# Performance work log

Measured on AMD Instinct MI355X. Metric: run time of the kernel, lower is better.

## Reference

```python
import jax, jax.numpy as jnp
import numpy as np

# --- the 9 fixed 3x3x3 planar structuring elements from MorphPool3D.__init__ ---
def _make_offsets():
    P = [np.zeros((3, 3, 3), np.int8) for _ in range(9)]
    P[0][:, :, 1] = 1
    P[1][:, 1, :] = 1
    P[2][1, :, :] = 1
    P[3][:, [0, 1, 2], [0, 1, 2]] = 1
    P[4][:, [0, 1, 2], [2, 1, 0]] = 1
    P[5][[0, 1, 2], :, [0, 1, 2]] = 1
    P[6][[0, 1, 2], :, [2, 1, 0]] = 1
    P[7][[0, 1, 2], [0, 1, 2], :] = 1
    P[8][[0, 1, 2], [2, 1, 0], :] = 1
    # list of [9,3] integer offsets relative to the 3x3x3 center (all masks are
    # point-symmetric, so scipy's structure reflection in dilation is a no-op)
    return [np.argwhere(m) - 1 for m in P]

_OFFSETS = _make_offsets()


def _morph_chain(x, red):
    """Sequentially apply all 9 structuring elements with reduction `red`.

    red = jnp.minimum -> composed binary erosions (scipy border_value=0 -> pad 0)
    red = jnp.maximum -> composed binary dilations (border_value=0   -> pad 0)
    Note: the original appends the SAME (in-place mutated) numpy array each
    iteration, so its max/min over 'layers' is a no-op; the net effect is the
    sequential composition over all 9 masks, which is what we compute here.
    x: [B, 1, D, H, W] binary float.
    """
    D, H, W = x.shape[-3:]
    for offs in _OFFSETS:
        xp = jnp.pad(x, ((0, 0), (0, 0), (1, 1), (1, 1), (1, 1)))  # zeros
        acc = None
        for di, dj, dk in offs:
            s = xp[:, :, 1 + di:1 + di + D, 1 + dj:1 + dj + H, 1 + dk:1 + dk + W]
            acc = s if acc is None else red(acc, s)
        x = acc
    return x


def _forward(inp, aux):
    # aux thresholding (MorphPoolFunction.forward), then binarize (scipy
    # binary_erosion/dilation treat any nonzero as True)
    t = jnp.where(aux < 0, jnp.ones((), inp.dtype),
                  jnp.where(aux > 0, jnp.zeros((), inp.dtype), inp))
    b = (t != 0).astype(inp.dtype)
    # Fcycle alternates per batch element starting at index 0:
    #   even i: inf_sup(sup_inf(x)) = erode_all(dilate_all(x))  (close-like)
    #   odd  i: sup_inf(inf_sup(x)) = dilate_all(erode_all(x))  (open-like)
    close = _morph_chain(_morph_chain(b, jnp.maximum), jnp.minimum)
    open_ = _morph_chain(_morph_chain(b, jnp.minimum), jnp.maximum)
    B = inp.shape[0]
    even = (jnp.arange(B) % 2 == 0).reshape(B, 1, 1, 1, 1)
    return jnp.where(even, close, open_)


def setup_inputs() -> dict:
    key = jax.random.key(0)
    k1, k2 = jax.random.split(key)
    B, C, D, H, W = 4, 1, 160, 160, 160
    inp = jax.random.uniform(k1, (B, C, D, H, W), dtype=jnp.float32)
    aux = jax.random.normal(k2, (B, C, D, H, W), dtype=jnp.float32)
    return {"input": inp, "aux": aux, "device": 0}


def reference(input, aux, device):
    del device  # CUDA device id in the original; irrelevant here
    return _forward(input, aux)
```

## Files before the change

### kernel.cpp

```cpp
#include <hip/hip_runtime.h>
#include <cstdint>

typedef unsigned long long u64;

constexpr int S   = 160;
constexpr int NB  = 4;
constexpr int PAD = 8;
constexpr int SP  = S + 2 * PAD;
constexpr int BUFW = NB * SP * 3 * SP;
constexpr int BLKC = 512;

__device__ __forceinline__ int widx(int b, int dp, int w, int hp) {
  return ((b * SP + dp) * 3 + w) * SP + hp;
}

struct R3 { u64 a, b, c; };

template <bool OR_> __device__ __forceinline__ u64 rop(u64 x, u64 y) { return OR_ ? (x | y) : (x & y); }
template <bool OR_> __device__ __forceinline__ R3 rop3(R3 x, R3 y) {
  return {rop<OR_>(x.a, y.a), rop<OR_>(x.b, y.b), rop<OR_>(x.c, y.c)};
}
template <int N> __device__ __forceinline__ R3 sl3(R3 x) {
  return {x.a << N, (x.b << N) | (x.a >> (64 - N)), (x.c << N) | (x.b >> (64 - N))};
}
template <int N> __device__ __forceinline__ R3 sr3(R3 x) {
  return {(x.a >> N) | (x.b << (64 - N)), (x.b >> N) | (x.c << (64 - N)), x.c >> N};
}
template <bool OR_> __device__ __forceinline__ R3 e1(R3 x) {
  return rop3<OR_>(rop3<OR_>(x, sl3<1>(x)), sr3<1>(x));
}
__device__ __forceinline__ R3 ldr(const u64* p) { return {p[0], p[1], p[2]}; }

template <bool OR_, bool TOOUT>
__device__ void chain_body(const u64* __restrict__ src, u64* __restrict__ dstBits,
                           float* __restrict__ out, int b, int d0, int h0,
                           u64* sIN, u64* sT1, u64* sT2) {
  for (int i = threadIdx.x; i < 32 * 32 * 3; i += BLKC) {
    const int hi = i % 32, w = (i / 32) % 3, di = i / 96;
    sIN[(di * 32 + hi) * 3 + w] = src[widx(b, d0 + di, w, h0 + hi)];
  }
  __syncthreads();

  for (int s = threadIdx.x; s < 32 * 20; s += BLKC) {
    const int dd = s / 20, hh = s % 20;
    const u64* base = sIN + (dd * 32 + hh) * 3;
    R3 G1 = ldr(base + 2 * 3);
#pragma unroll
    for (int r = 3; r <= 10; ++r) G1 = rop3<OR_>(G1, ldr(base + r * 3));
    R3 G2 = rop3<OR_>(ldr(base + 1 * 3), ldr(base + 11 * 3));
    R3 G3 = rop3<OR_>(ldr(base + 0 * 3), ldr(base + 12 * 3));
    R3 X = rop3<OR_>(rop3<OR_>(e1<OR_>(e1<OR_>(G1)), e1<OR_>(G2)), G3);
    R3 y = e1<OR_>(X);
    R3 R = rop3<OR_>(rop3<OR_>(y, sl3<3>(y)), sr3<3>(y));
    R.c &= 0xFFFFFFFFull;
    u64* q = sT1 + s * 3; q[0] = R.a; q[1] = R.b; q[2] = R.c;
  }
  __syncthreads();

  for (int s = threadIdx.x; s < 20 * 20; s += BLKC) {
    const int dd = s / 20, hh = s % 20;
    const u64* base = sT1 + (dd * 20 + hh) * 3;
    R3 G1 = ldr(base + 2 * 60);
#pragma unroll
    for (int r = 3; r <= 10; ++r) G1 = rop3<OR_>(G1, ldr(base + r * 60));
    R3 G2 = rop3<OR_>(ldr(base + 1 * 60), ldr(base + 11 * 60));
    R3 G3 = rop3<OR_>(ldr(base + 0 * 60), ldr(base + 12 * 60));
    R3 X = rop3<OR_>(e1<OR_>(rop3<OR_>(e1<OR_>(G1), G2)), G3);
    X.c &= 0xFFFFFFFFull;
    u64* q = sT2 + s * 3; q[0] = X.a; q[1] = X.b; q[2] = X.c;
  }
  __syncthreads();

  if (threadIdx.x < 256) {
    const int s = threadIdx.x;
    const int dd = s >> 4, hh = s & 15;
    const u64* t2 = sT2 + ((dd + 2) * 20 + (hh + 2)) * 3;
    R3 A = ldr(t2);
    A = rop3<OR_>(A, ldr(t2 + (20 + 1) * 3));  A = rop3<OR_>(A, ldr(t2 + (20 - 1) * 3));
    A = rop3<OR_>(A, ldr(t2 - (20 - 1) * 3));  A = rop3<OR_>(A, ldr(t2 - (20 + 1) * 3));
    A = rop3<OR_>(A, ldr(t2 + 40 * 3));        A = rop3<OR_>(A, ldr(t2 - 40 * 3));
    A = rop3<OR_>(A, ldr(t2 + 2 * 3));         A = rop3<OR_>(A, ldr(t2 - 2 * 3));
    A.c &= 0xFFFFFFFFull;
    if (TOOUT) {
      u64* q = sT1 + s * 3;
      q[0] = A.a; q[1] = A.b; q[2] = A.c;
    } else {
      dstBits[widx(b, d0 + dd + PAD, 0, h0 + hh + PAD)] = A.a;
      dstBits[widx(b, d0 + dd + PAD, 1, h0 + hh + PAD)] = A.b;
      dstBits[widx(b, d0 + dd + PAD, 2, h0 + hh + PAD)] = A.c;
    }
  }
  if (TOOUT) {
    __syncthreads();
    for (int q = threadIdx.x; q < 16 * 16 * 40; q += BLKC) {
      const int r = q / 40, j = q % 40;
      const int dd = r >> 4, hh = r & 15;
      const u64 word = sT1[r * 3 + (j >> 4)];
      const unsigned nb = (unsigned)((word >> ((j & 15) * 4)) & 0xFull);
      float4 v;
      v.x = (float)(nb & 1u); v.y = (float)((nb >> 1) & 1u);
      v.z = (float)((nb >> 2) & 1u); v.w = (float)((nb >> 3) & 1u);
      const size_t e = ((size_t)((b * S + d0 + dd) * S + h0 + hh)) * S + j * 4;
      *reinterpret_cast<float4*>(out + e) = v;
    }
  }
}

template <bool PH0, bool TOOUT>
__global__ __launch_bounds__(BLKC) void chain_k(const u64* __restrict__ src,
                                                u64* __restrict__ dstBits,
                                                float* __restrict__ out) {
  __shared__ u64 sIN[32 * 32 * 3];
  __shared__ u64 sT1[32 * 20 * 3];
  __shared__ u64 sT2[20 * 20 * 3];
  const int blk = blockIdx.x;
  const int b = blk / 100, tile = blk % 100;
  const int d0 = (tile / 10) * 16, h0 = (tile % 10) * 16;
  const bool isor = (((b & 1) == 0) == PH0);
  if (isor) chain_body<true , TOOUT>(src, dstBits, out, b, d0, h0, sIN, sT1, sT2);
  else      chain_body<false, TOOUT>(src, dstBits, out, b, d0, h0, sIN, sT1, sT2);
}

__device__ __forceinline__ u64 squash(u64 x) {
  x = (x | (x >> 4))  & 0x00FF00FF00FF00FFull;
  x = (x | (x >> 8))  & 0x0000FFFF0000FFFFull;
  x = (x | (x >> 16)) & 0x00000000FFFFFFFFull;
  return x;
}

__global__ __launch_bounds__(320) void pack_k(const float* __restrict__ aux,
                                              const float* __restrict__ inp,
                                              u64* __restrict__ dstA,
                                              u64* __restrict__ dstB) {
  {
    const int g = blockIdx.x * 320 + threadIdx.x;
    if (g < BUFW) {
      const int hp = g % SP;
      const int dp = (g / (SP * 3)) % SP;
      if ((dp < PAD) | (dp >= S + PAD) | (hp < PAD) | (hp >= S + PAD)) {
        dstA[g] = 0ull; dstB[g] = 0ull;
      }
    }
  }
  __shared__ unsigned char nib[8][48];
  const int r   = threadIdx.x / 40;
  const int pos = threadIdx.x % 40;
  const int row = blockIdx.x * 8 + r;
  const size_t ebase = (size_t)row * S + pos * 4;

  const float4 a = reinterpret_cast<const float4*>(aux)[row * 40 + pos];
  unsigned n = 0;
  if (a.x < 0.0f) n |= 1u; else if (a.x == 0.0f) { if (inp[ebase + 0] != 0.0f) n |= 1u; }
  if (a.y < 0.0f) n |= 2u; else if (a.y == 0.0f) { if (inp[ebase + 1] != 0.0f) n |= 2u; }
  if (a.z < 0.0f) n |= 4u; else if (a.z == 0.0f) { if (inp[ebase + 2] != 0.0f) n |= 4u; }
  if (a.w < 0.0f) n |= 8u; else if (a.w == 0.0f) { if (inp[ebase + 3] != 0.0f) n |= 8u; }
  nib[r][pos] = (unsigned char)n;
  if (threadIdx.x < 64) nib[threadIdx.x >> 3][40 + (threadIdx.x & 7)] = 0;
  __syncthreads();

  if (threadIdx.x < 24) {
    const int rr = threadIdx.x & 7;
    const int w  = threadIdx.x >> 3;
    const u64 x0 = *reinterpret_cast<const u64*>(&nib[rr][w * 16]);
    const u64 x1 = *reinterpret_cast<const u64*>(&nib[rr][w * 16 + 8]);
    const u64 word = squash(x0) | (squash(x1) << 32);
    const int grow = blockIdx.x * 8 + rr;
    const int h = grow % S, d = (grow / S) % S, b = grow / (S * S);
    dstA[widx(b, d + PAD, w, h + PAD)] = word;
  }
}

extern "C" void kernel_launch(void* const* d_in, const int* in_sizes, int n_in,
                              void* d_out, int out_size, void* d_ws, size_t ws_size,
                              hipStream_t stream) {
  (void)in_sizes; (void)n_in; (void)out_size; (void)ws_size;
  const float* inp = (const float*)d_in[0];
  const float* aux = (const float*)d_in[1];
  float* out = (float*)d_out;

  u64* bufA = (u64*)d_ws;
  u64* bufB = bufA + BUFW;

  const int ROWS = NB * S * S;
  pack_k<<<ROWS / 8, 320, 0, stream>>>(aux, inp, bufA, bufB);

  const int CG = NB * 100;
  chain_k<true , false><<<CG, BLKC, 0, stream>>>(bufA, bufB, out);
  chain_k<false, true ><<<CG, BLKC, 0, stream>>>(bufB, bufA, out);
}
```

Measured before the change: 41.19 us.

## Fuse both morphology chain passes into one kernel with a grid barrier

The two chain kernels are merged into one persistent kernel. It runs the first chain, synchronizes all 400 blocks through an atomic counter grid barrier, then runs the second chain. The counter is zeroed inside the pack kernel. This removes one kernel launch and its launch gap. It also switches the aux load and the float output store to nontemporal accesses. The barrier only works if all 400 blocks of 512 threads are co-resident, which holds on MI355X's 256 CUs with the occupancy hint, but a spinning barrier risks deadlock if that fails.

```diff
diff --git a/kernel.cpp b/kernel.cpp
--- a/kernel.cpp
+++ b/kernel.cpp
@@ -2,6 +2,7 @@
 #include <cstdint>
 
 typedef unsigned long long u64;
+typedef float f4 __attribute__((ext_vector_type(4)));
 
 constexpr int S   = 160;
 constexpr int NB  = 4;
@@ -9,6 +10,7 @@
 constexpr int SP  = S + 2 * PAD;
 constexpr int BUFW = NB * SP * 3 * SP;
 constexpr int BLKC = 512;
+constexpr int GRIDC = NB * 100;
 
 __device__ __forceinline__ int widx(int b, int dp, int w, int hp) {
   return ((b * SP + dp) * 3 + w) * SP + hp;
@@ -97,28 +99,44 @@
       const int dd = r >> 4, hh = r & 15;
       const u64 word = sT1[r * 3 + (j >> 4)];
       const unsigned nb = (unsigned)((word >> ((j & 15) * 4)) & 0xFull);
-      float4 v;
+      f4 v;
       v.x = (float)(nb & 1u); v.y = (float)((nb >> 1) & 1u);
       v.z = (float)((nb >> 2) & 1u); v.w = (float)((nb >> 3) & 1u);
       const size_t e = ((size_t)((b * S + d0 + dd) * S + h0 + hh)) * S + j * 4;
-      *reinterpret_cast<float4*>(out + e) = v;
-    }
-  }
-}
-
-template <bool PH0, bool TOOUT>
-__global__ __launch_bounds__(BLKC) void chain_k(const u64* __restrict__ src,
-                                                u64* __restrict__ dstBits,
-                                                float* __restrict__ out) {
+      __builtin_nontemporal_store(v, reinterpret_cast<f4*>(out + e));
+    }
+  }
+}
+
+__global__ __launch_bounds__(BLKC, 4) void mega_k(const u64* __restrict__ bufA,
+                                                  u64* __restrict__ bufB,
+                                                  float* __restrict__ out,
+                                                  unsigned* __restrict__ cnt) {
   __shared__ u64 sIN[32 * 32 * 3];
   __shared__ u64 sT1[32 * 20 * 3];
   __shared__ u64 sT2[20 * 20 * 3];
   const int blk = blockIdx.x;
   const int b = blk / 100, tile = blk % 100;
   const int d0 = (tile / 10) * 16, h0 = (tile % 10) * 16;
-  const bool isor = (((b & 1) == 0) == PH0);
-  if (isor) chain_body<true , TOOUT>(src, dstBits, out, b, d0, h0, sIN, sT1, sT2);
-  else      chain_body<false, TOOUT>(src, dstBits, out, b, d0, h0, sIN, sT1, sT2);
+
+  const bool isorA = ((b & 1) == 0);
+  if (isorA) chain_body<true , false>(bufA, bufB, out, b, d0, h0, sIN, sT1, sT2);
+  else       chain_body<false, false>(bufA, bufB, out, b, d0, h0, sIN, sT1, sT2);
+
+  __syncthreads();
+  if (threadIdx.x == 0) {
+    __threadfence();
+    __hip_atomic_fetch_add(cnt, 1u, __ATOMIC_ACQ_REL, __HIP_MEMORY_SCOPE_AGENT);
+    while (__hip_atomic_load(cnt, __ATOMIC_RELAXED, __HIP_MEMORY_SCOPE_AGENT) < (unsigned)GRIDC) {
+      __builtin_amdgcn_s_sleep(8);
+    }
+    __threadfence();
+  }
+  __syncthreads();
+
+  const bool isorB = ((b & 1) != 0);
+  if (isorB) chain_body<true , true>(bufB, nullptr, out, b, d0, h0, sIN, sT1, sT2);
+  else       chain_body<false, true>(bufB, nullptr, out, b, d0, h0, sIN, sT1, sT2);
 }
 
 __device__ __forceinline__ u64 squash(u64 x) {
@@ -131,9 +149,11 @@
 __global__ __launch_bounds__(320) void pack_k(const float* __restrict__ aux,
                                               const float* __restrict__ inp,
                                               u64* __restrict__ dstA,
-                                              u64* __restrict__ dstB) {
+                                              u64* __restrict__ dstB,
+                                              unsigned* __restrict__ cnt) {
   {
     const int g = blockIdx.x * 320 + threadIdx.x;
+    if (g == 0) *cnt = 0u;
     if (g < BUFW) {
       const int hp = g % SP;
       const int dp = (g / (SP * 3)) % SP;
@@ -148,7 +168,7 @@
   const int row = blockIdx.x * 8 + r;
   const size_t ebase = (size_t)row * S + pos * 4;
 
-  const float4 a = reinterpret_cast<const float4*>(aux)[row * 40 + pos];
+  const f4 a = __builtin_nontemporal_load(reinterpret_cast<const f4*>(aux) + (row * 40 + pos));
   unsigned n = 0;
   if (a.x < 0.0f) n |= 1u; else if (a.x == 0.0f) { if (inp[ebase + 0] != 0.0f) n |= 1u; }
   if (a.y < 0.0f) n |= 2u; else if (a.y == 0.0f) { if (inp[ebase + 1] != 0.0f) n |= 2u; }
@@ -180,11 +200,10 @@
 
   u64* bufA = (u64*)d_ws;
   u64* bufB = bufA + BUFW;
+  unsigned* cnt = (unsigned*)(bufB + BUFW);
 
   const int ROWS = NB * S * S;
-  pack_k<<<ROWS / 8, 320, 0, stream>>>(aux, inp, bufA, bufB);
-
-  const int CG = NB * 100;
-  chain_k<true , false><<<CG, BLKC, 0, stream>>>(bufA, bufB, out);
-  chain_k<false, true ><<<CG, BLKC, 0, stream>>>(bufB, bufA, out);
-}
+  pack_k<<<ROWS / 8, 320, 0, stream>>>(aux, inp, bufA, bufB, cnt);
+
+  mega_k<<<GRIDC, BLKC, 0, stream>>>(bufA, bufB, out, cnt);
+}
```

Result: slower. 92.04 us (+123.4%).

## Fuse bit-packing with first H-axis morphology pass into per-slice kernel

Applied to the files above, without the earlier changes.

Packing the thresholded input into bitmasks now happens in a per-(batch, depth-slice) kernel that also runs the first H-direction stage of the first morphology chain directly from shared memory. The remaining D-direction and planar stages of that chain become a lighter tiled kernel that only loads a 32x20 halo instead of 32x32. The float output uses nontemporal stores and the aux reads use nontemporal loads. This removes one intermediate shared-memory pass and part of the halo reload, but the pack kernel now runs at the coarser grid of 640 blocks of 256 threads.

```diff
diff --git a/kernel.cpp b/kernel.cpp
--- a/kernel.cpp
+++ b/kernel.cpp
@@ -2,6 +2,7 @@
 #include <cstdint>
 
 typedef unsigned long long u64;
+typedef float f4 __attribute__((ext_vector_type(4)));
 
 constexpr int S   = 160;
 constexpr int NB  = 4;
@@ -31,10 +32,131 @@
 }
 __device__ __forceinline__ R3 ldr(const u64* p) { return {p[0], p[1], p[2]}; }
 
-template <bool OR_, bool TOOUT>
-__device__ void chain_body(const u64* __restrict__ src, u64* __restrict__ dstBits,
-                           float* __restrict__ out, int b, int d0, int h0,
-                           u64* sIN, u64* sT1, u64* sT2) {
+__device__ __forceinline__ u64 squash(u64 x) {
+  x = (x | (x >> 4))  & 0x00FF00FF00FF00FFull;
+  x = (x | (x >> 8))  & 0x0000FFFF0000FFFFull;
+  x = (x | (x >> 16)) & 0x00000000FFFFFFFFull;
+  return x;
+}
+
+template <bool OR_>
+__device__ void p1_slice(const u64* __restrict__ bits, u64* __restrict__ dstA, int b, int d) {
+  for (int hh = threadIdx.x; hh < S; hh += 256) {
+    const u64* base = bits + (hh + 6) * 3;
+    R3 G1 = ldr(base - 4 * 3);
+#pragma unroll
+    for (int r = -3; r <= 4; ++r) G1 = rop3<OR_>(G1, ldr(base + r * 3));
+    R3 G2 = rop3<OR_>(ldr(base - 5 * 3), ldr(base + 5 * 3));
+    R3 G3 = rop3<OR_>(ldr(base - 6 * 3), ldr(base + 6 * 3));
+    R3 X = rop3<OR_>(rop3<OR_>(e1<OR_>(e1<OR_>(G1)), e1<OR_>(G2)), G3);
+    R3 y = e1<OR_>(X);
+    R3 Rr = rop3<OR_>(rop3<OR_>(y, sl3<3>(y)), sr3<3>(y));
+    Rr.c &= 0xFFFFFFFFull;
+    dstA[widx(b, d + PAD, 0, hh + PAD)] = Rr.a;
+    dstA[widx(b, d + PAD, 1, hh + PAD)] = Rr.b;
+    dstA[widx(b, d + PAD, 2, hh + PAD)] = Rr.c;
+  }
+}
+
+__global__ __launch_bounds__(256) void packp1_k(const float* __restrict__ aux,
+                                                const float* __restrict__ inp,
+                                                u64* __restrict__ bufA,
+                                                u64* __restrict__ bufB) {
+  __shared__ unsigned char nib[160][48];
+  __shared__ u64 bits[172 * 3];
+  const int blk = blockIdx.x;
+  const int b = blk / S, d = blk % S;
+  const int tid = threadIdx.x;
+
+  for (int g = blk * 256 + tid; g < BUFW; g += 640 * 256) {
+    const int hp = g % SP;
+    const int dp = (g / (SP * 3)) % SP;
+    if ((dp < PAD) | (dp >= S + PAD) | (hp < PAD) | (hp >= S + PAD)) { bufA[g] = 0ull; bufB[g] = 0ull; }
+  }
+
+  for (int i = tid; i < 36; i += 256) {
+    const int r = i / 3, w = i % 3;
+    const int row = (r < 6) ? r : 160 + r;
+    bits[row * 3 + w] = 0ull;
+  }
+  for (int i = tid; i < 160 * 8; i += 256) nib[i >> 3][40 + (i & 7)] = 0;
+
+  const f4* srcp = reinterpret_cast<const f4*>(aux) + (size_t)(b * S + d) * 6400;
+  const size_t eb0 = (size_t)(b * S + d) * 25600;
+  for (int i = tid; i < 6400; i += 256) {
+    const f4 a = __builtin_nontemporal_load(srcp + i);
+    unsigned n = 0;
+    if (a.x < 0.0f) n |= 1u; else if (a.x == 0.0f) { if (inp[eb0 + i * 4 + 0] != 0.0f) n |= 1u; }
+    if (a.y < 0.0f) n |= 2u; else if (a.y == 0.0f) { if (inp[eb0 + i * 4 + 1] != 0.0f) n |= 2u; }
+    if (a.z < 0.0f) n |= 4u; else if (a.z == 0.0f) { if (inp[eb0 + i * 4 + 2] != 0.0f) n |= 4u; }
+    if (a.w < 0.0f) n |= 8u; else if (a.w == 0.0f) { if (inp[eb0 + i * 4 + 3] != 0.0f) n |= 8u; }
+    nib[i / 40][i % 40] = (unsigned char)n;
+  }
+  __syncthreads();
+  for (int t = tid; t < 480; t += 256) {
+    const int row = t / 3, w = t % 3;
+    const u64 x0 = *reinterpret_cast<const u64*>(&nib[row][w * 16]);
+    const u64 x1 = *reinterpret_cast<const u64*>(&nib[row][w * 16 + 8]);
+    bits[(row + 6) * 3 + w] = squash(x0) | (squash(x1) << 32);
+  }
+  __syncthreads();
+
+  if ((b & 1) == 0) p1_slice<true >(bits, bufA, b, d);
+  else              p1_slice<false>(bits, bufA, b, d);
+}
+
+template <bool OR_>
+__device__ void p23_body(const u64* __restrict__ src, u64* __restrict__ dst,
+                         int b, int d0, int h0, u64* sIN, u64* sT2) {
+  for (int i = threadIdx.x; i < 32 * 20 * 3; i += BLKC) {
+    const int hi = i % 20, w = (i / 20) % 3, di = i / 60;
+    sIN[(di * 20 + hi) * 3 + w] = src[widx(b, d0 + di, w, h0 + hi + 6)];
+  }
+  __syncthreads();
+
+  for (int s = threadIdx.x; s < 20 * 20; s += BLKC) {
+    const int dd = s / 20, hh = s % 20;
+    const u64* base = sIN + (dd * 20 + hh) * 3;
+    R3 G1 = ldr(base + 2 * 60);
+#pragma unroll
+    for (int r = 3; r <= 10; ++r) G1 = rop3<OR_>(G1, ldr(base + r * 60));
+    R3 G2 = rop3<OR_>(ldr(base + 1 * 60), ldr(base + 11 * 60));
+    R3 G3 = rop3<OR_>(ldr(base + 0 * 60), ldr(base + 12 * 60));
+    R3 X = rop3<OR_>(e1<OR_>(rop3<OR_>(e1<OR_>(G1), G2)), G3);
+    X.c &= 0xFFFFFFFFull;
+    u64* q = sT2 + s * 3; q[0] = X.a; q[1] = X.b; q[2] = X.c;
+  }
+  __syncthreads();
+
+  if (threadIdx.x < 256) {
+    const int dd = threadIdx.x >> 4, hh = threadIdx.x & 15;
+    const u64* t2 = sT2 + ((dd + 2) * 20 + (hh + 2)) * 3;
+    R3 A = ldr(t2);
+    A = rop3<OR_>(A, ldr(t2 + 21 * 3)); A = rop3<OR_>(A, ldr(t2 + 19 * 3));
+    A = rop3<OR_>(A, ldr(t2 - 19 * 3)); A = rop3<OR_>(A, ldr(t2 - 21 * 3));
+    A = rop3<OR_>(A, ldr(t2 + 40 * 3)); A = rop3<OR_>(A, ldr(t2 - 40 * 3));
+    A = rop3<OR_>(A, ldr(t2 + 2 * 3));  A = rop3<OR_>(A, ldr(t2 - 2 * 3));
+    A.c &= 0xFFFFFFFFull;
+    dst[widx(b, d0 + dd + PAD, 0, h0 + hh + PAD)] = A.a;
+    dst[widx(b, d0 + dd + PAD, 1, h0 + hh + PAD)] = A.b;
+    dst[widx(b, d0 + dd + PAD, 2, h0 + hh + PAD)] = A.c;
+  }
+}
+
+__global__ __launch_bounds__(BLKC) void p23_k(const u64* __restrict__ src,
+                                              u64* __restrict__ dst) {
+  __shared__ u64 sIN[32 * 20 * 3];
+  __shared__ u64 sT2[20 * 20 * 3];
+  const int blk = blockIdx.x;
+  const int b = blk / 100, tile = blk % 100;
+  const int d0 = (tile / 10) * 16, h0 = (tile % 10) * 16;
+  if ((b & 1) == 0) p23_body<true >(src, dst, b, d0, h0, sIN, sT2);
+  else              p23_body<false>(src, dst, b, d0, h0, sIN, sT2);
+}
+
+template <bool OR_>
+__device__ void chain_body(const u64* __restrict__ src, float* __restrict__ out,
+                           int b, int d0, int h0, u64* sIN, u64* sT1, u64* sT2) {
   for (int i = threadIdx.x; i < 32 * 32 * 3; i += BLKC) {
     const int hi = i % 32, w = (i / 32) % 3, di = i / 96;
     sIN[(di * 32 + hi) * 3 + w] = src[widx(b, d0 + di, w, h0 + hi)];
@@ -76,98 +198,39 @@
     const int dd = s >> 4, hh = s & 15;
     const u64* t2 = sT2 + ((dd + 2) * 20 + (hh + 2)) * 3;
     R3 A = ldr(t2);
-    A = rop3<OR_>(A, ldr(t2 + (20 + 1) * 3));  A = rop3<OR_>(A, ldr(t2 + (20 - 1) * 3));
-    A = rop3<OR_>(A, ldr(t2 - (20 - 1) * 3));  A = rop3<OR_>(A, ldr(t2 - (20 + 1) * 3));
-    A = rop3<OR_>(A, ldr(t2 + 40 * 3));        A = rop3<OR_>(A, ldr(t2 - 40 * 3));
-    A = rop3<OR_>(A, ldr(t2 + 2 * 3));         A = rop3<OR_>(A, ldr(t2 - 2 * 3));
+    A = rop3<OR_>(A, ldr(t2 + 21 * 3)); A = rop3<OR_>(A, ldr(t2 + 19 * 3));
+    A = rop3<OR_>(A, ldr(t2 - 19 * 3)); A = rop3<OR_>(A, ldr(t2 - 21 * 3));
+    A = rop3<OR_>(A, ldr(t2 + 40 * 3)); A = rop3<OR_>(A, ldr(t2 - 40 * 3));
+    A = rop3<OR_>(A, ldr(t2 + 2 * 3));  A = rop3<OR_>(A, ldr(t2 - 2 * 3));
     A.c &= 0xFFFFFFFFull;
-    if (TOOUT) {
-      u64* q = sT1 + s * 3;
-      q[0] = A.a; q[1] = A.b; q[2] = A.c;
-    } else {
-      dstBits[widx(b, d0 + dd + PAD, 0, h0 + hh + PAD)] = A.a;
-      dstBits[widx(b, d0 + dd + PAD, 1, h0 + hh + PAD)] = A.b;
-      dstBits[widx(b, d0 + dd + PAD, 2, h0 + hh + PAD)] = A.c;
-    }
-  }
-  if (TOOUT) {
-    __syncthreads();
-    for (int q = threadIdx.x; q < 16 * 16 * 40; q += BLKC) {
-      const int r = q / 40, j = q % 40;
-      const int dd = r >> 4, hh = r & 15;
-      const u64 word = sT1[r * 3 + (j >> 4)];
-      const unsigned nb = (unsigned)((word >> ((j & 15) * 4)) & 0xFull);
-      float4 v;
-      v.x = (float)(nb & 1u); v.y = (float)((nb >> 1) & 1u);
-      v.z = (float)((nb >> 2) & 1u); v.w = (float)((nb >> 3) & 1u);
-      const size_t e = ((size_t)((b * S + d0 + dd) * S + h0 + hh)) * S + j * 4;
-      *reinterpret_cast<float4*>(out + e) = v;
-    }
-  }
-}
-
-template <bool PH0, bool TOOUT>
-__global__ __launch_bounds__(BLKC) void chain_k(const u64* __restrict__ src,
-                                                u64* __restrict__ dstBits,
-                                                float* __restrict__ out) {
+    u64* q = sT1 + s * 3;
+    q[0] = A.a; q[1] = A.b; q[2] = A.c;
+  }
+  __syncthreads();
+
+  for (int q = threadIdx.x; q < 16 * 16 * 40; q += BLKC) {
+    const int r = q / 40, j = q % 40;
+    const int dd = r >> 4, hh = r & 15;
+    const u64 word = sT1[r * 3 + (j >> 4)];
+    const unsigned nb = (unsigned)((word >> ((j & 15) * 4)) & 0xFull);
+    f4 v;
+    v.x = (float)(nb & 1u); v.y = (float)((nb >> 1) & 1u);
+    v.z = (float)((nb >> 2) & 1u); v.w = (float)((nb >> 3) & 1u);
+    const size_t e = ((size_t)((b * S + d0 + dd) * S + h0 + hh)) * S + j * 4;
+    __builtin_nontemporal_store(v, reinterpret_cast<f4*>(out + e));
+  }
+}
+
+__global__ __launch_bounds__(BLKC) void chain2_k(const u64* __restrict__ src,
+                                                 float* __restrict__ out) {
   __shared__ u64 sIN[32 * 32 * 3];
   __shared__ u64 sT1[32 * 20 * 3];
   __shared__ u64 sT2[20 * 20 * 3];
   const int blk = blockIdx.x;
   const int b = blk / 100, tile = blk % 100;
   const int d0 = (tile / 10) * 16, h0 = (tile % 10) * 16;
-  const bool isor = (((b & 1) == 0) == PH0);
-  if (isor) chain_body<true , TOOUT>(src, dstBits, out, b, d0, h0, sIN, sT1, sT2);
-  else      chain_body<false, TOOUT>(src, dstBits, out, b, d0, h0, sIN, sT1, sT2);
-}
-
-__device__ __forceinline__ u64 squash(u64 x) {
-  x = (x | (x >> 4))  & 0x00FF00FF00FF00FFull;
-  x = (x | (x >> 8))  & 0x0000FFFF0000FFFFull;
-  x = (x | (x >> 16)) & 0x00000000FFFFFFFFull;
-  return x;
-}
-
-__global__ __launch_bounds__(320) void pack_k(const float* __restrict__ aux,
-                                              const float* __restrict__ inp,
-                                              u64* __restrict__ dstA,
-                                              u64* __restrict__ dstB) {
-  {
-    const int g = blockIdx.x * 320 + threadIdx.x;
-    if (g < BUFW) {
-      const int hp = g % SP;
-      const int dp = (g / (SP * 3)) % SP;
-      if ((dp < PAD) | (dp >= S + PAD) | (hp < PAD) | (hp >= S + PAD)) {
-        dstA[g] = 0ull; dstB[g] = 0ull;
-      }
-    }
-  }
-  __shared__ unsigned char nib[8][48];
-  const int r   = threadIdx.x / 40;
-  const int pos = threadIdx.x % 40;
-  const int row = blockIdx.x * 8 + r;
-  const size_t ebase = (size_t)row * S + pos * 4;
-
-  const float4 a = reinterpret_cast<const float4*>(aux)[row * 40 + pos];
-  unsigned n = 0;
-  if (a.x < 0.0f) n |= 1u; else if (a.x == 0.0f) { if (inp[ebase + 0] != 0.0f) n |= 1u; }
-  if (a.y < 0.0f) n |= 2u; else if (a.y == 0.0f) { if (inp[ebase + 1] != 0.0f) n |= 2u; }
-  if (a.z < 0.0f) n |= 4u; else if (a.z == 0.0f) { if (inp[ebase + 2] != 0.0f) n |= 4u; }
-  if (a.w < 0.0f) n |= 8u; else if (a.w == 0.0f) { if (inp[ebase + 3] != 0.0f) n |= 8u; }
-  nib[r][pos] = (unsigned char)n;
-  if (threadIdx.x < 64) nib[threadIdx.x >> 3][40 + (threadIdx.x & 7)] = 0;
-  __syncthreads();
-
-  if (threadIdx.x < 24) {
-    const int rr = threadIdx.x & 7;
-    const int w  = threadIdx.x >> 3;
-    const u64 x0 = *reinterpret_cast<const u64*>(&nib[rr][w * 16]);
-    const u64 x1 = *reinterpret_cast<const u64*>(&nib[rr][w * 16 + 8]);
-    const u64 word = squash(x0) | (squash(x1) << 32);
-    const int grow = blockIdx.x * 8 + rr;
-    const int h = grow % S, d = (grow / S) % S, b = grow / (S * S);
-    dstA[widx(b, d + PAD, w, h + PAD)] = word;
-  }
+  if ((b & 1) != 0) chain_body<true >(src, out, b, d0, h0, sIN, sT1, sT2);
+  else              chain_body<false>(src, out, b, d0, h0, sIN, sT1, sT2);
 }
 
 extern "C" void kernel_launch(void* const* d_in, const int* in_sizes, int n_in,
@@ -181,10 +244,7 @@
   u64* bufA = (u64*)d_ws;
   u64* bufB = bufA + BUFW;
 
-  const int ROWS = NB * S * S;
-  pack_k<<<ROWS / 8, 320, 0, stream>>>(aux, inp, bufA, bufB);
-
-  const int CG = NB * 100;
-  chain_k<true , false><<<CG, BLKC, 0, stream>>>(bufA, bufB, out);
-  chain_k<false, true ><<<CG, BLKC, 0, stream>>>(bufB, bufA, out);
-}
+  packp1_k<<<NB * S, 256, 0, stream>>>(aux, inp, bufA, bufB);
+  p23_k<<<NB * 100, BLKC, 0, stream>>>(bufA, bufB);
+  chain2_k<<<NB * 100, BLKC, 0, stream>>>(bufB, out);
+}
```

Result: slower. 52.65 us (+27.8%).
